# Kernel optimization log

Hardware: AMD Instinct MI355X
Metric: run time of the kernel (lower is better)

Reference implementation:

```python
import jax, jax.numpy as jnp
import numpy as np


def setup_inputs() -> dict:
    key = jax.random.key(0)
    k1, k2, k3, k4, k5, k6 = jax.random.split(key, 6)
    B, N, K = 2, 60000, 16
    C_in, C_add, C_mid = 64, 3, 16
    out_features = 128
    in_features = (C_in + C_add) * C_mid  # 1072
    return {
        "input_features": jax.random.normal(k1, (B, N, C_in), dtype=jnp.float32),
        "neighbor_inds": jax.random.randint(k2, (B, N, K), 0, N, dtype=jnp.int32),
        "weightnet": jax.random.normal(k3, (B, N, K, C_mid), dtype=jnp.float32),
        "additional_features": jax.random.normal(k4, (B, N, K, C_add), dtype=jnp.float32),
        "linear_weight": jax.random.normal(k5, (out_features, in_features), dtype=jnp.float32) * 0.03,
        "linear_bias": jax.random.normal(k6, (out_features,), dtype=jnp.float32),
    }


def reference(input_features, neighbor_inds, weightnet, additional_features, linear_weight, linear_bias):
    # Gather neighbor features: [B, N, K, C_in]
    gathered = jax.vmap(lambda feats, idx: feats[idx])(input_features, neighbor_inds)
    # Concat per-neighbor additional features: [B, N, K, C_in + C_add]
    feat = jnp.concatenate([gathered, additional_features], axis=-1)
    # PConv: contract over neighbors K against weightnet -> [B, N, C, M]
    pconv = jnp.einsum('bnkc,bnkm->bncm', feat, weightnet)
    B, N = pconv.shape[0], pconv.shape[1]
    pconv = pconv.reshape(B, N, -1)  # [B, N, (C_in+C_add)*C_mid]
    # Fused linear projection
    return jnp.einsum('bnf,of->bno', pconv, linear_weight) + linear_bias
```

## Files before the change

kernel.cpp:

```cpp
#include <hip/hip_runtime.h>

#define NPTS  60000
#define NBLK  1875
#define FP    1088
#define PSTR  1096
#define SPBYTES (32 * PSTR * 2)

typedef _Float16 f16x4 __attribute__((ext_vector_type(4)));
typedef _Float16 f16x8 __attribute__((ext_vector_type(8)));
typedef float    f32x4 __attribute__((ext_vector_type(4)));

__global__ void __launch_bounds__(256)
cvt_lw_kernel(const float* __restrict__ LW, _Float16* __restrict__ LWh) {
    const int o = blockIdx.x;
    for (int f = threadIdx.x; f < FP; f += 256) {
        const float v = (f < 1072) ? LW[o * 1072 + f] : 0.f;
        LWh[(f >> 5) * (128 * 32) + o * 32 + (f & 31)] = (_Float16)v;
    }
}

struct GRegs {
    float fv[4][4];
    float wv[4];
    float av[4];
};

static __device__ __forceinline__ void issue_gather(
    const float* __restrict__ inF, const float* __restrict__ Wn,
    const float* __restrict__ addF, int bbase, int base_nk,
    int ind_lane, int i, int q, int ml, bool mlo, GRegs& g)
{
    #pragma unroll
    for (int j = 0; j < 4; ++j) {
        const int k   = q * 4 + j;
        const int idx = __shfl(ind_lane, i * 16 + k, 64);
        const float* fp = inF + (bbase + idx) * 64 + ml;
        #pragma unroll
        for (int ct = 0; ct < 4; ++ct)
            g.fv[ct][j] = fp[ct * 16];
        g.wv[j] = Wn[(base_nk + k) * 16 + ml];
        g.av[j] = mlo ? addF[(base_nk + k) * 3 + ml] : 0.f;
    }
}

static __device__ __forceinline__ void compute_point(
    const GRegs& g, _Float16* sProw, int qsw, int ml, bool mlo)
{
    const f32x4 z4 = {0.f, 0.f, 0.f, 0.f};
    f16x4 aW, bA;
    #pragma unroll
    for (int j = 0; j < 4; ++j) { aW[j] = (_Float16)g.wv[j]; bA[j] = (_Float16)g.av[j]; }

    #pragma unroll
    for (int ct = 0; ct < 4; ++ct) {
        f16x4 bF;
        #pragma unroll
        for (int j = 0; j < 4; ++j) bF[j] = (_Float16)g.fv[ct][j];
        const f32x4 d = __builtin_amdgcn_mfma_f32_16x16x16f16(aW, bF, z4, 0, 0, 0);
        f16x4 dh;
        #pragma unroll
        for (int r = 0; r < 4; ++r) dh[r] = (_Float16)d[r];
        *(f16x4*)&sProw[(ct * 16 + ml) * 16 + qsw * 4] = dh;
    }
    const f32x4 d = __builtin_amdgcn_mfma_f32_16x16x16f16(aW, bA, z4, 0, 0, 0);
    if (mlo) {
        f16x4 dh;
        #pragma unroll
        for (int r = 0; r < 4; ++r) dh[r] = (_Float16)d[r];
        *(f16x4*)&sProw[(64 + ml) * 16 + qsw * 4] = dh;
    }
}

__global__ void __launch_bounds__(512, 4)
pconv_linear_mfma(const float* __restrict__ inF,
                  const int*   __restrict__ inds,
                  const float* __restrict__ Wn,
                  const float* __restrict__ addF,
                  const _Float16* __restrict__ LWh,
                  const float* __restrict__ bias,
                  float*       __restrict__ out)
{
    extern __shared__ __align__(16) _Float16 sP[];

    const int t    = threadIdx.x;
    const int lane = t & 63;
    const int w    = t >> 6;
    const int q    = lane >> 4;
    const int ml   = lane & 15;
    const bool mlo = (ml < 3);
    const int qsw  = q ^ (((ml >> 2) & 1) << 1);

    const int bid   = blockIdx.x;
    const int b     = bid / NBLK;
    const int n0    = (bid - b * NBLK) * 32;
    const int bbase = b * NPTS;

    const int ind_lane = inds[(bbase + n0 + w * 4) * 16 + lane];

    sP[(t >> 4) * PSTR + 1072 + (t & 15)] = (_Float16)0.f;

    const int nk0 = (bbase + n0 + w * 4) * 16;
    _Float16* sPw = sP + (w * 4) * PSTR;
    GRegs g0, g1;
    issue_gather(inF, Wn, addF, bbase, nk0,      ind_lane, 0, q, ml, mlo, g0);
    issue_gather(inF, Wn, addF, bbase, nk0 + 16, ind_lane, 1, q, ml, mlo, g1);
    compute_point(g0, sPw,            qsw, ml, mlo);
    issue_gather(inF, Wn, addF, bbase, nk0 + 32, ind_lane, 2, q, ml, mlo, g0);
    compute_point(g1, sPw + PSTR,     qsw, ml, mlo);
    issue_gather(inF, Wn, addF, bbase, nk0 + 48, ind_lane, 3, q, ml, mlo, g1);
    compute_point(g0, sPw + 2 * PSTR, qsw, ml, mlo);
    compute_point(g1, sPw + 3 * PSTR, qsw, ml, mlo);
    __syncthreads();

    const int o0 = w * 16;
    const float bz = bias[o0 + ml];
    f32x4 acc0 = {0.f, 0.f, 0.f, 0.f};
    f32x4 acc1 = {0.f, 0.f, 0.f, 0.f};
    const _Float16* aP0 = sP + ml * PSTR + (q >> 1) * 16 + (q & 1) * 8;
    const _Float16* aP1 = aP0 + 16 * PSTR;
    const int flip = (q & 1) ? -8 : 8;
    const _Float16* bP = LWh + (o0 + ml) * 32 + q * 8;

    #pragma unroll 2
    for (int ch = 0; ch < 34; ++ch) {
        const int off = ch * 32 + ((ch & 2) ? flip : 0);
        f16x8 bf = *(const f16x8*)(bP + ch * 4096);
        f16x8 a0 = *(const f16x8*)(aP0 + off);
        f16x8 a1 = *(const f16x8*)(aP1 + off);
        acc0 = __builtin_amdgcn_mfma_f32_16x16x32_f16(a0, bf, acc0, 0, 0, 0);
        acc1 = __builtin_amdgcn_mfma_f32_16x16x32_f16(a1, bf, acc1, 0, 0, 0);
    }

    float* ob = out + (bbase + n0 + q * 4) * 128 + o0 + ml;
    #pragma unroll
    for (int r = 0; r < 4; ++r)
        ob[r * 128] = acc0[r] + bz;
    ob += 16 * 128;
    #pragma unroll
    for (int r = 0; r < 4; ++r)
        ob[r * 128] = acc1[r] + bz;
}

extern "C" void kernel_launch(void* const* d_in, const int* in_sizes, int n_in,
                              void* d_out, int out_size, void* d_ws, size_t ws_size,
                              hipStream_t stream)
{
    const float* inF  = (const float*)d_in[0];
    const int*   inds = (const int*)  d_in[1];
    const float* Wn   = (const float*)d_in[2];
    const float* addF = (const float*)d_in[3];
    const float* LW   = (const float*)d_in[4];
    const float* bias = (const float*)d_in[5];
    float* out = (float*)d_out;
    _Float16* LWh = (_Float16*)d_ws;

    hipFuncSetAttribute((const void*)pconv_linear_mfma,
                        hipFuncAttributeMaxDynamicSharedMemorySize, SPBYTES);

    cvt_lw_kernel<<<dim3(128), dim3(256), 0, stream>>>(LW, LWh);
    pconv_linear_mfma<<<dim3(2 * NBLK), dim3(512), SPBYTES, stream>>>(
        inF, inds, Wn, addF, LWh, bias, out);
}
```

Baseline: 346.2 us.

## Pre-convert gathered features to fp16 with vectorized layout and prefetch weights

Adds a pre-pass that converts input features to fp16 in a channel-interleaved layout, so each lane can gather one 8-byte vector per neighbor instead of four scalar fp32 loads. This halves gather bytes and cuts the number of load instructions. All four gather groups are now issued before any compute, and the linear weights are register-prefetched two chunks ahead across the barrier. The cost is an extra conversion kernel pass over the inputs, more register pressure, and a fallback path used when the workspace is too small.

```diff
diff --git a/kernel.cpp b/kernel.cpp
--- a/kernel.cpp
+++ b/kernel.cpp
@@ -5,6 +5,9 @@
 #define FP    1088
 #define PSTR  1096
 #define SPBYTES (32 * PSTR * 2)
+#define LWH_BYTES   (128 * FP * 2)
+#define INF16_BYTES (2 * NPTS * 64 * 2)
+#define WS_NEED     (LWH_BYTES + INF16_BYTES)
 
 typedef _Float16 f16x4 __attribute__((ext_vector_type(4)));
 typedef _Float16 f16x8 __attribute__((ext_vector_type(8)));
@@ -19,16 +22,38 @@
     }
 }
 
-struct GRegs {
-    float fv[4][4];
-    float wv[4];
-    float av[4];
-};
-
-static __device__ __forceinline__ void issue_gather(
+__global__ void __launch_bounds__(256)
+cvt_inf_kernel(const float* __restrict__ inF, _Float16* __restrict__ inF16) {
+    const int tid = blockIdx.x * 256 + threadIdx.x;
+    if (tid >= 2 * NPTS * 64) return;
+    const int c = tid & 63;
+    const int n = tid >> 6;
+    inF16[(n << 6) + ((c & 15) << 2) + (c >> 4)] = (_Float16)inF[tid];
+}
+
+template<bool F16P> struct GRegs;
+template<> struct GRegs<true>  { f16x4 fv[4];    float wv[4]; float av[4]; };
+template<> struct GRegs<false> { float fv[4][4]; float wv[4]; float av[4]; };
+
+static __device__ __forceinline__ void issue_gather16(
+    const _Float16* __restrict__ inF16, const float* __restrict__ Wn,
+    const float* __restrict__ addF, int bbase, int base_nk,
+    int ind_lane, int i, int q, int ml, bool mlo, GRegs<true>& g)
+{
+    #pragma unroll
+    for (int j = 0; j < 4; ++j) {
+        const int k   = q * 4 + j;
+        const int idx = __shfl(ind_lane, i * 16 + k, 64);
+        g.fv[j] = *(const f16x4*)(inF16 + (bbase + idx) * 64 + ml * 4);
+        g.wv[j] = Wn[(base_nk + k) * 16 + ml];
+        g.av[j] = mlo ? addF[(base_nk + k) * 3 + ml] : 0.f;
+    }
+}
+
+static __device__ __forceinline__ void issue_gather32(
     const float* __restrict__ inF, const float* __restrict__ Wn,
     const float* __restrict__ addF, int bbase, int base_nk,
-    int ind_lane, int i, int q, int ml, bool mlo, GRegs& g)
+    int ind_lane, int i, int q, int ml, bool mlo, GRegs<false>& g)
 {
     #pragma unroll
     for (int j = 0; j < 4; ++j) {
@@ -43,8 +68,9 @@
     }
 }
 
+template<bool F16P>
 static __device__ __forceinline__ void compute_point(
-    const GRegs& g, _Float16* sProw, int qsw, int ml, bool mlo)
+    const GRegs<F16P>& g, _Float16* sProw, int qsw, int ml, bool mlo)
 {
     const f32x4 z4 = {0.f, 0.f, 0.f, 0.f};
     f16x4 aW, bA;
@@ -55,7 +81,10 @@
     for (int ct = 0; ct < 4; ++ct) {
         f16x4 bF;
         #pragma unroll
-        for (int j = 0; j < 4; ++j) bF[j] = (_Float16)g.fv[ct][j];
+        for (int j = 0; j < 4; ++j) {
+            if constexpr (F16P) bF[j] = g.fv[j][ct];
+            else                bF[j] = (_Float16)g.fv[ct][j];
+        }
         const f32x4 d = __builtin_amdgcn_mfma_f32_16x16x16f16(aW, bF, z4, 0, 0, 0);
         f16x4 dh;
         #pragma unroll
@@ -71,8 +100,10 @@
     }
 }
 
+template<bool F16P>
 __global__ void __launch_bounds__(512, 4)
 pconv_linear_mfma(const float* __restrict__ inF,
+                  const _Float16* __restrict__ inF16,
                   const int*   __restrict__ inds,
                   const float* __restrict__ Wn,
                   const float* __restrict__ addF,
@@ -101,34 +132,51 @@
 
     const int nk0 = (bbase + n0 + w * 4) * 16;
     _Float16* sPw = sP + (w * 4) * PSTR;
-    GRegs g0, g1;
-    issue_gather(inF, Wn, addF, bbase, nk0,      ind_lane, 0, q, ml, mlo, g0);
-    issue_gather(inF, Wn, addF, bbase, nk0 + 16, ind_lane, 1, q, ml, mlo, g1);
-    compute_point(g0, sPw,            qsw, ml, mlo);
-    issue_gather(inF, Wn, addF, bbase, nk0 + 32, ind_lane, 2, q, ml, mlo, g0);
-    compute_point(g1, sPw + PSTR,     qsw, ml, mlo);
-    issue_gather(inF, Wn, addF, bbase, nk0 + 48, ind_lane, 3, q, ml, mlo, g1);
-    compute_point(g0, sPw + 2 * PSTR, qsw, ml, mlo);
-    compute_point(g1, sPw + 3 * PSTR, qsw, ml, mlo);
+    if constexpr (F16P) {
+        GRegs<true> g0, g1, g2, g3;
+        issue_gather16(inF16, Wn, addF, bbase, nk0,      ind_lane, 0, q, ml, mlo, g0);
+        issue_gather16(inF16, Wn, addF, bbase, nk0 + 16, ind_lane, 1, q, ml, mlo, g1);
+        issue_gather16(inF16, Wn, addF, bbase, nk0 + 32, ind_lane, 2, q, ml, mlo, g2);
+        issue_gather16(inF16, Wn, addF, bbase, nk0 + 48, ind_lane, 3, q, ml, mlo, g3);
+        compute_point<true>(g0, sPw,            qsw, ml, mlo);
+        compute_point<true>(g1, sPw + PSTR,     qsw, ml, mlo);
+        compute_point<true>(g2, sPw + 2 * PSTR, qsw, ml, mlo);
+        compute_point<true>(g3, sPw + 3 * PSTR, qsw, ml, mlo);
+    } else {
+        GRegs<false> g0, g1;
+        issue_gather32(inF, Wn, addF, bbase, nk0,      ind_lane, 0, q, ml, mlo, g0);
+        issue_gather32(inF, Wn, addF, bbase, nk0 + 16, ind_lane, 1, q, ml, mlo, g1);
+        compute_point<false>(g0, sPw,            qsw, ml, mlo);
+        issue_gather32(inF, Wn, addF, bbase, nk0 + 32, ind_lane, 2, q, ml, mlo, g0);
+        compute_point<false>(g1, sPw + PSTR,     qsw, ml, mlo);
+        issue_gather32(inF, Wn, addF, bbase, nk0 + 48, ind_lane, 3, q, ml, mlo, g1);
+        compute_point<false>(g0, sPw + 2 * PSTR, qsw, ml, mlo);
+        compute_point<false>(g1, sPw + 3 * PSTR, qsw, ml, mlo);
+    }
+
+    const int o0 = w * 16;
+    const _Float16* bP = LWh + (o0 + ml) * 32 + q * 8;
+    f16x8 bcur = *(const f16x8*)(bP);
+    f16x8 bnxt = *(const f16x8*)(bP + 4096);
     __syncthreads();
 
-    const int o0 = w * 16;
     const float bz = bias[o0 + ml];
     f32x4 acc0 = {0.f, 0.f, 0.f, 0.f};
     f32x4 acc1 = {0.f, 0.f, 0.f, 0.f};
     const _Float16* aP0 = sP + ml * PSTR + (q >> 1) * 16 + (q & 1) * 8;
     const _Float16* aP1 = aP0 + 16 * PSTR;
     const int flip = (q & 1) ? -8 : 8;
-    const _Float16* bP = LWh + (o0 + ml) * 32 + q * 8;
 
     #pragma unroll 2
     for (int ch = 0; ch < 34; ++ch) {
+        const int chf = (ch + 2 < 34) ? (ch + 2) : 33;
+        f16x8 bfut = *(const f16x8*)(bP + chf * 4096);
         const int off = ch * 32 + ((ch & 2) ? flip : 0);
-        f16x8 bf = *(const f16x8*)(bP + ch * 4096);
         f16x8 a0 = *(const f16x8*)(aP0 + off);
         f16x8 a1 = *(const f16x8*)(aP1 + off);
-        acc0 = __builtin_amdgcn_mfma_f32_16x16x32_f16(a0, bf, acc0, 0, 0, 0);
-        acc1 = __builtin_amdgcn_mfma_f32_16x16x32_f16(a1, bf, acc1, 0, 0, 0);
+        acc0 = __builtin_amdgcn_mfma_f32_16x16x32_f16(a0, bcur, acc0, 0, 0, 0);
+        acc1 = __builtin_amdgcn_mfma_f32_16x16x32_f16(a1, bcur, acc1, 0, 0, 0);
+        bcur = bnxt; bnxt = bfut;
     }
 
     float* ob = out + (bbase + n0 + q * 4) * 128 + o0 + ml;
@@ -154,10 +202,22 @@
     float* out = (float*)d_out;
     _Float16* LWh = (_Float16*)d_ws;
 
-    hipFuncSetAttribute((const void*)pconv_linear_mfma,
+    const bool f16p = (ws_size >= (size_t)WS_NEED);
+
+    hipFuncSetAttribute((const void*)pconv_linear_mfma<true>,
                         hipFuncAttributeMaxDynamicSharedMemorySize, SPBYTES);
+    hipFuncSetAttribute((const void*)pconv_linear_mfma<false>,
+                        hipFuncAttributeMaxDynamicSharedMemorySize, SPBYTES);
 
     cvt_lw_kernel<<<dim3(128), dim3(256), 0, stream>>>(LW, LWh);
-    pconv_linear_mfma<<<dim3(2 * NBLK), dim3(512), SPBYTES, stream>>>(
-        inF, inds, Wn, addF, LWh, bias, out);
-}
+    if (f16p) {
+        _Float16* inF16 = (_Float16*)((char*)d_ws + LWH_BYTES);
+        cvt_inf_kernel<<<dim3((2 * NPTS * 64 + 255) / 256), dim3(256), 0, stream>>>(
+            inF, inF16);
+        pconv_linear_mfma<true><<<dim3(2 * NBLK), dim3(512), SPBYTES, stream>>>(
+            inF, inF16, inds, Wn, addF, LWh, bias, out);
+    } else {
+        pconv_linear_mfma<false><<<dim3(2 * NBLK), dim3(512), SPBYTES, stream>>>(
+            inF, (const _Float16*)nullptr, inds, Wn, addF, LWh, bias, out);
+    }
+}
```

New measurement: 362.4 us. +4.7%, slower.
